# Optimization experiments

Measured on AMD Instinct MI355X. Metric: run time of the kernel, lower is better.

## Reference

```python
import jax, jax.numpy as jnp
import numpy as np

IN_DIM = 768
ATT_DIM = 512
N_HEADS = 8
HEAD_DIM = ATT_DIM // N_HEADS


def setup_inputs() -> dict:
    key = jax.random.key(0)
    k1, k2, k3 = jax.random.split(key, 3)
    X = jax.random.normal(k1, (4, 2048, IN_DIM), dtype=jnp.float32)
    # qkv linear (no bias): weight [3*att_dim, in_dim], torch convention y = x W^T
    W_qkv = jax.random.normal(k2, (3 * ATT_DIM, IN_DIM), dtype=jnp.float32) * (1.0 / np.sqrt(IN_DIM))
    W_out = jax.random.normal(k3, (IN_DIM, ATT_DIM), dtype=jnp.float32) * (1.0 / np.sqrt(ATT_DIM))
    b_out = jnp.zeros((IN_DIM,), dtype=jnp.float32)
    return {"X": X, "W_qkv": W_qkv, "W_out": W_out, "b_out": b_out}


def reference(X, W_qkv, W_out, b_out):
    b, n, _ = X.shape
    QKV = jnp.einsum('bnf,cf->bnc', X, W_qkv)  # [b, n, 3*att_dim]
    # rearrange 'b n (p h d) -> p b h n d'
    QKV = QKV.reshape(b, n, 3, N_HEADS, HEAD_DIM).transpose(2, 0, 3, 1, 4)
    Q, K, V = QKV[0], QKV[1], QKV[2]  # each [b, h, n, d]
    scores = jnp.einsum('bhid,bhjd->bhij', Q, K) / np.sqrt(HEAD_DIM)
    A = jax.nn.softmax(scores, axis=-1)  # dropout p=0 -> identity
    Y = jnp.einsum('bhij,bhjd->bhid', A, V)
    Y = Y.transpose(0, 2, 1, 3).reshape(b, n, ATT_DIM)  # 'b h n d -> b n (h d)'
    return jnp.einsum('bna,oa->bno', Y, W_out) + b_out
```

## Files before the change

### kernel.cpp

```cpp
#include <hip/hip_runtime.h>

typedef __bf16 bf16;
typedef unsigned int u32;
typedef __attribute__((ext_vector_type(8))) __bf16 bf16x8;
typedef __attribute__((ext_vector_type(4))) __bf16 bf16x4;
typedef __attribute__((ext_vector_type(4))) float floatx4;

#define IN_DIM  768
#define ATT_DIM 512
#define NH      8
#define HD      64
#define BATCH   4
#define SEQ     2048
#define M_TOT   (BATCH*SEQ)
#define QKV_N   (3*ATT_DIM)

#define QSCALE 0.18033688011112042f

__device__ __forceinline__ void cp16(void* lds, const void* g) {
    __builtin_amdgcn_global_load_lds((const __attribute__((address_space(1))) u32*)g,
                                     (__attribute__((address_space(3))) u32*)lds, 16, 0, 0);
}
__device__ __forceinline__ const bf16* swz(const bf16* b, int row, int chunk) {
    return b + row * 64 + (((chunk) ^ (row & 7)) << 3);
}

#define N8_X  (M_TOT * IN_DIM / 8)
#define N8_WQ (QKV_N * IN_DIM / 8)
#define N8_WO (IN_DIM * ATT_DIM / 8)
#define N8_ALL (N8_X + N8_WQ + N8_WO)

__global__ __launch_bounds__(256) void cvt_all(const float* __restrict__ X,
                                               const float* __restrict__ Wq,
                                               const float* __restrict__ Wo,
                                               bf16* __restrict__ Xb,
                                               bf16* __restrict__ Wqb,
                                               bf16* __restrict__ Wob) {
    int i = blockIdx.x * 256 + threadIdx.x;
    const float* s; bf16* d; int off;
    if (i < N8_X)            { s = X;  d = Xb;  off = i; }
    else if (i < N8_X+N8_WQ) { s = Wq; d = Wqb; off = i - N8_X; }
    else                     { s = Wo; d = Wob; off = i - N8_X - N8_WQ; }
    const float4 a = ((const float4*)s)[2*off];
    const float4 b = ((const float4*)s)[2*off+1];
    bf16x8 o = {(bf16)a.x,(bf16)a.y,(bf16)a.z,(bf16)a.w,
                (bf16)b.x,(bf16)b.y,(bf16)b.z,(bf16)b.w};
    ((bf16x8*)d)[off] = o;
}

__global__ __launch_bounds__(256) void qkv_gemm(const bf16* __restrict__ Xb,
                                                const bf16* __restrict__ Wb,
                                                bf16* __restrict__ Q,
                                                bf16* __restrict__ Kv,
                                                bf16* __restrict__ VT) {
    __shared__ __align__(16) char smraw[34816];
    bf16* As = (bf16*)smraw;
    bf16* Bs = (bf16*)(smraw + 16384);

    const int tid  = threadIdx.x;
    const int bm0  = blockIdx.y * 128;
    const int bn0  = blockIdx.x * 128;
    const int wave = tid >> 6, lane = tid & 63;
    const int quad = lane >> 4, l15 = lane & 15;
    const int wm = (wave >> 1) * 64, wn = (wave & 1) * 64;
    const int r8 = lane >> 3, cc = (lane & 7) ^ r8;

    const bf16* ag = Xb + (size_t)(bm0 + wave * 32 + r8) * IN_DIM + cc * 8;
    const bf16* bg = Wb + (size_t)(bn0 + wave * 32 + r8) * IN_DIM + cc * 8;

    floatx4 acc[4][4];
#pragma unroll
    for (int i = 0; i < 4; ++i)
#pragma unroll
        for (int j = 0; j < 4; ++j) acc[i][j] = (floatx4){0.f, 0.f, 0.f, 0.f};

    for (int kt = 0; kt < IN_DIM / 64; ++kt) {
        __syncthreads();
#pragma unroll
        for (int it = 0; it < 4; ++it) {
            cp16(&As[(wave * 32 + it * 8) * 64], ag + it * (8 * IN_DIM) + kt * 64);
            cp16(&Bs[(wave * 32 + it * 8) * 64], bg + it * (8 * IN_DIM) + kt * 64);
        }
        __syncthreads();

        bf16x8 af[2][4], bfr[2][4];
#pragma unroll
        for (int kh = 0; kh < 2; ++kh)
#pragma unroll
            for (int i = 0; i < 4; ++i) {
                af[kh][i]  = *(const bf16x8*)swz(As, wm + i * 16 + l15, kh * 4 + quad);
                bfr[kh][i] = *(const bf16x8*)swz(Bs, wn + i * 16 + l15, kh * 4 + quad);
            }
#pragma unroll
        for (int kh = 0; kh < 2; ++kh)
#pragma unroll
            for (int i = 0; i < 4; ++i)
#pragma unroll
                for (int j = 0; j < 4; ++j)
                    acc[i][j] = __builtin_amdgcn_mfma_f32_16x16x32_bf16(af[kh][i], bfr[kh][j], acc[i][j], 0, 0, 0);
    }

    const int b = bm0 >> 11, nbase = bm0 & 2047;

    if (bn0 < 1024) {
#pragma unroll
        for (int i = 0; i < 4; ++i)
#pragma unroll
            for (int j = 0; j < 4; ++j)
#pragma unroll
                for (int r = 0; r < 4; ++r) {
                    const int row = bm0 + wm + i * 16 + quad * 4 + r;
                    const int col = bn0 + wn + j * 16 + l15;
                    const float v = acc[i][j][r];
                    const int rem = col & 511;
                    const int h = rem >> 6, d = rem & 63;
                    const int n = row & 2047;
                    const size_t idx = (((size_t)((row >> 11) * NH + h)) * SEQ + n) * HD + d;
                    if (col < 512) Q[idx]  = (bf16)(v * QSCALE);
                    else           Kv[idx] = (bf16)v;
                }
    } else {
        __syncthreads();
        bf16 (*Ts)[136] = (bf16(*)[136])smraw;
#pragma unroll
        for (int i = 0; i < 4; ++i)
#pragma unroll
            for (int j = 0; j < 4; ++j) {
                bf16x4 pk = {(bf16)acc[i][j][0], (bf16)acc[i][j][1],
                             (bf16)acc[i][j][2], (bf16)acc[i][j][3]};
                *(bf16x4*)&Ts[wn + j * 16 + l15][wm + i * 16 + quad * 4] = pk;
            }
        __syncthreads();
        const int cb = bn0 - 1024;
#pragma unroll
        for (int t2 = 0; t2 < 8; ++t2) {
            const int id = tid + t2 * 256;
            const int c = id >> 4, nc = (id & 15) * 8;
            const int col = cb + c;
            const int h = col >> 6, d = col & 63;
            *(bf16x8*)&VT[(((size_t)(b * NH + h)) * HD + d) * SEQ + nbase + nc] =
                *(const bf16x8*)&Ts[c][nc];
        }
    }
}

__global__ __launch_bounds__(256, 4) void attn(const bf16* __restrict__ Q,
                                               const bf16* __restrict__ K,
                                               const bf16* __restrict__ VT,
                                               bf16* __restrict__ Y) {
    __shared__ bf16 Ks[2][64 * 64];
    __shared__ bf16 VTs[2][64 * 64];
    __shared__ bf16 Ps[4][16 * 64];

    const int tid  = threadIdx.x;
    const int wave = tid >> 6, lane = tid & 63;
    const int quad = lane >> 4, l15 = lane & 15;
    const int bh = blockIdx.x;
    const int q0 = blockIdx.y * 64;
    const bf16* Qg = Q  + (size_t)bh * SEQ * HD;
    const bf16* Kg = K  + (size_t)bh * SEQ * HD;
    const bf16* Vg = VT + (size_t)bh * HD * SEQ;

    const int r8 = lane >> 3, cc = (lane & 7) ^ r8;

    bf16x8 aq[2];
    aq[0] = *(const bf16x8*)&Qg[(size_t)(q0 + wave * 16 + l15) * 64 + quad * 8];
    aq[1] = *(const bf16x8*)&Qg[(size_t)(q0 + wave * 16 + l15) * 64 + 32 + quad * 8];

    const bf16* kg0 = Kg + (size_t)(wave * 16 + r8) * 64 + cc * 8;
    const bf16* kg1 = Kg + (size_t)(wave * 16 + 8 + r8) * 64 + cc * 8;
    const bf16* vg0 = Vg + (size_t)(wave * 16 + r8) * 2048 + cc * 8;
    const bf16* vg1 = Vg + (size_t)(wave * 16 + 8 + r8) * 2048 + cc * 8;

    cp16(&Ks[0][(wave * 16) * 64], kg0);
    cp16(&Ks[0][(wave * 16 + 8) * 64], kg1);
    cp16(&VTs[0][(wave * 16) * 64], vg0);
    cp16(&VTs[0][(wave * 16 + 8) * 64], vg1);

    float l = 0.f;
    floatx4 o[4];
#pragma unroll
    for (int db = 0; db < 4; ++db) o[db] = (floatx4){0.f, 0.f, 0.f, 0.f};

    bf16* psw = &Ps[wave][0];

    for (int kt = 0; kt < SEQ / 64; ++kt) {
        const int cur = kt & 1, nb = cur ^ 1;
        __syncthreads();
        if (kt < SEQ / 64 - 1) {
            cp16(&Ks[nb][(wave * 16) * 64], kg0 + (size_t)(kt + 1) * 4096);
            cp16(&Ks[nb][(wave * 16 + 8) * 64], kg1 + (size_t)(kt + 1) * 4096);
            cp16(&VTs[nb][(wave * 16) * 64], vg0 + (kt + 1) * 64);
            cp16(&VTs[nb][(wave * 16 + 8) * 64], vg1 + (kt + 1) * 64);
        }

#pragma unroll
        for (int t = 0; t < 4; ++t) {
            const int kr = t * 16 + l15;
            const bf16x8 k0 = *(const bf16x8*)swz(Ks[cur], kr, quad);
            const bf16x8 k1 = *(const bf16x8*)swz(Ks[cur], kr, 4 + quad);
            floatx4 z = (floatx4){0.f, 0.f, 0.f, 0.f};
            z = __builtin_amdgcn_mfma_f32_16x16x32_bf16(k0, aq[0], z, 0, 0, 0);
            z = __builtin_amdgcn_mfma_f32_16x16x32_bf16(k1, aq[1], z, 0, 0, 0);
            const float p0 = __builtin_amdgcn_exp2f(z[0]);
            const float p1 = __builtin_amdgcn_exp2f(z[1]);
            const float p2 = __builtin_amdgcn_exp2f(z[2]);
            const float p3 = __builtin_amdgcn_exp2f(z[3]);
            l += (p0 + p1) + (p2 + p3);
            bf16x4 pk = {(bf16)p0, (bf16)p1, (bf16)p2, (bf16)p3};
            const int c = t * 2 + (quad >> 1);
            *(bf16x4*)&psw[l15 * 64 + ((c ^ (l15 & 7)) << 3) + ((quad & 1) << 2)] = pk;
        }
        const bf16x8 pa0 = *(const bf16x8*)swz(psw, l15, quad);
        const bf16x8 pa1 = *(const bf16x8*)swz(psw, l15, 4 + quad);

#pragma unroll
        for (int db = 0; db < 4; ++db) {
            const int vr = db * 16 + l15;
            const bf16x8 v0 = *(const bf16x8*)swz(VTs[cur], vr, quad);
            const bf16x8 v1 = *(const bf16x8*)swz(VTs[cur], vr, 4 + quad);
            o[db] = __builtin_amdgcn_mfma_f32_16x16x32_bf16(pa0, v0, o[db], 0, 0, 0);
            o[db] = __builtin_amdgcn_mfma_f32_16x16x32_bf16(pa1, v1, o[db], 0, 0, 0);
        }
    }

    l += __shfl_xor(l, 16, 64);
    l += __shfl_xor(l, 32, 64);
    const float inv = 1.0f / l;
    float linv[4];
#pragma unroll
    for (int r = 0; r < 4; ++r)
        linv[r] = __int_as_float(__builtin_amdgcn_ds_bpermute((quad * 4 + r) * 4,
                                                              __float_as_int(inv)));
    const int b = bh >> 3, h = bh & 7;
#pragma unroll
    for (int db = 0; db < 4; ++db)
#pragma unroll
        for (int r = 0; r < 4; ++r) {
            const int n = q0 + wave * 16 + quad * 4 + r;
            Y[((size_t)(b * SEQ + n)) * ATT_DIM + h * HD + db * 16 + l15] =
                (bf16)(o[db][r] * linv[r]);
        }
}

__global__ __launch_bounds__(256) void out_gemm(const bf16* __restrict__ Yb,
                                                const bf16* __restrict__ Wb,
                                                const float* __restrict__ bias,
                                                float* __restrict__ out) {
    __shared__ __align__(16) bf16 As[128 * 64];
    __shared__ __align__(16) bf16 Bs[128 * 64];

    const int tid  = threadIdx.x;
    const int bm0  = blockIdx.y * 128;
    const int bn0  = blockIdx.x * 128;
    const int wave = tid >> 6, lane = tid & 63;
    const int quad = lane >> 4, l15 = lane & 15;
    const int wm = (wave >> 1) * 64, wn = (wave & 1) * 64;
    const int r8 = lane >> 3, cc = (lane & 7) ^ r8;

    const bf16* ag = Yb + (size_t)(bm0 + wave * 32 + r8) * ATT_DIM + cc * 8;
    const bf16* bg = Wb + (size_t)(bn0 + wave * 32 + r8) * ATT_DIM + cc * 8;

    floatx4 acc[4][4];
#pragma unroll
    for (int i = 0; i < 4; ++i)
#pragma unroll
        for (int j = 0; j < 4; ++j) acc[i][j] = (floatx4){0.f, 0.f, 0.f, 0.f};

    for (int kt = 0; kt < ATT_DIM / 64; ++kt) {
        __syncthreads();
#pragma unroll
        for (int it = 0; it < 4; ++it) {
            cp16(&As[(wave * 32 + it * 8) * 64], ag + it * (8 * ATT_DIM) + kt * 64);
            cp16(&Bs[(wave * 32 + it * 8) * 64], bg + it * (8 * ATT_DIM) + kt * 64);
        }
        __syncthreads();

        bf16x8 af[2][4], bfr[2][4];
#pragma unroll
        for (int kh = 0; kh < 2; ++kh)
#pragma unroll
            for (int i = 0; i < 4; ++i) {
                af[kh][i]  = *(const bf16x8*)swz(As, wm + i * 16 + l15, kh * 4 + quad);
                bfr[kh][i] = *(const bf16x8*)swz(Bs, wn + i * 16 + l15, kh * 4 + quad);
            }
#pragma unroll
        for (int kh = 0; kh < 2; ++kh)
#pragma unroll
            for (int i = 0; i < 4; ++i)
#pragma unroll
                for (int j = 0; j < 4; ++j)
                    acc[i][j] = __builtin_amdgcn_mfma_f32_16x16x32_bf16(af[kh][i], bfr[kh][j], acc[i][j], 0, 0, 0);
    }

#pragma unroll
    for (int i = 0; i < 4; ++i)
#pragma unroll
        for (int j = 0; j < 4; ++j)
#pragma unroll
            for (int r = 0; r < 4; ++r) {
                const int row = bm0 + wm + i * 16 + quad * 4 + r;
                const int col = bn0 + wn + j * 16 + l15;
                out[(size_t)row * IN_DIM + col] = acc[i][j][r] + bias[col];
            }
}

extern "C" void kernel_launch(void* const* d_in, const int* in_sizes, int n_in,
                              void* d_out, int out_size, void* d_ws, size_t ws_size,
                              hipStream_t stream) {
    const float* X    = (const float*)d_in[0];
    const float* Wqkv = (const float*)d_in[1];
    const float* Wout = (const float*)d_in[2];
    const float* bout = (const float*)d_in[3];
    float* out = (float*)d_out;

    char* ws = (char*)d_ws;
    size_t off = 0;
    bf16* Xb  = (bf16*)(ws + off); off += (size_t)M_TOT * IN_DIM * 2;
    bf16* Wqb = (bf16*)(ws + off); off += (size_t)QKV_N * IN_DIM * 2;
    bf16* Wob = (bf16*)(ws + off); off += (size_t)IN_DIM * ATT_DIM * 2;
    const size_t T = (size_t)BATCH * NH * SEQ * HD * 2;
    bf16* Q  = (bf16*)(ws + off); off += T;
    bf16* K  = (bf16*)(ws + off); off += T;
    bf16* VT = (bf16*)(ws + off); off += T;
    bf16* Y  = (bf16*)(ws + off); off += T;

    cvt_all<<<N8_ALL / 256, 256, 0, stream>>>(X, Wqkv, Wout, Xb, Wqb, Wob);
    qkv_gemm<<<dim3(QKV_N / 128, M_TOT / 128), 256, 0, stream>>>(Xb, Wqb, Q, K, VT);
    attn<<<dim3(BATCH * NH, SEQ / 64), 256, 0, stream>>>(Q, K, VT, Y);
    out_gemm<<<dim3(IN_DIM / 128, M_TOT / 128), 256, 0, stream>>>(Y, Wob, bout, out);
}
```

Measured before the change: 176.9 us.

## Process two query tiles per wave in attention; shrink out_gemm M tile

The attention kernel now gives each wave 32 query rows as two 16-row groups instead of 16, so every K and V^T tile staged in shared memory serves twice as many queries. This halves the grid and the global-to-LDS traffic for K/V per query. The cost is higher register pressure, with the launch-bounds occupancy hint lowered from 4 to 2 blocks per SM. Separately, out_gemm uses a 64x128 tile instead of 128x128, doubling its block count to give more parallelism on a small GEMM.

```diff
diff --git a/kernel.cpp b/kernel.cpp
--- a/kernel.cpp
+++ b/kernel.cpp
@@ -144,28 +144,32 @@
     }
 }
 
-__global__ __launch_bounds__(256, 4) void attn(const bf16* __restrict__ Q,
+__global__ __launch_bounds__(256, 2) void attn(const bf16* __restrict__ Q,
                                                const bf16* __restrict__ K,
                                                const bf16* __restrict__ VT,
                                                bf16* __restrict__ Y) {
     __shared__ bf16 Ks[2][64 * 64];
     __shared__ bf16 VTs[2][64 * 64];
-    __shared__ bf16 Ps[4][16 * 64];
+    __shared__ bf16 Ps[4][2][16 * 64];
 
     const int tid  = threadIdx.x;
     const int wave = tid >> 6, lane = tid & 63;
     const int quad = lane >> 4, l15 = lane & 15;
     const int bh = blockIdx.x;
-    const int q0 = blockIdx.y * 64;
+    const int q0 = blockIdx.y * 128;
     const bf16* Qg = Q  + (size_t)bh * SEQ * HD;
     const bf16* Kg = K  + (size_t)bh * SEQ * HD;
     const bf16* Vg = VT + (size_t)bh * HD * SEQ;
 
     const int r8 = lane >> 3, cc = (lane & 7) ^ r8;
 
-    bf16x8 aq[2];
-    aq[0] = *(const bf16x8*)&Qg[(size_t)(q0 + wave * 16 + l15) * 64 + quad * 8];
-    aq[1] = *(const bf16x8*)&Qg[(size_t)(q0 + wave * 16 + l15) * 64 + 32 + quad * 8];
+    bf16x8 aq[2][2];
+#pragma unroll
+    for (int g = 0; g < 2; ++g) {
+        const size_t qrow = (size_t)(q0 + wave * 32 + g * 16 + l15) * 64;
+        aq[g][0] = *(const bf16x8*)&Qg[qrow + quad * 8];
+        aq[g][1] = *(const bf16x8*)&Qg[qrow + 32 + quad * 8];
+    }
 
     const bf16* kg0 = Kg + (size_t)(wave * 16 + r8) * 64 + cc * 8;
     const bf16* kg1 = Kg + (size_t)(wave * 16 + 8 + r8) * 64 + cc * 8;
@@ -177,12 +181,12 @@
     cp16(&VTs[0][(wave * 16) * 64], vg0);
     cp16(&VTs[0][(wave * 16 + 8) * 64], vg1);
 
-    float l = 0.f;
-    floatx4 o[4];
-#pragma unroll
-    for (int db = 0; db < 4; ++db) o[db] = (floatx4){0.f, 0.f, 0.f, 0.f};
-
-    bf16* psw = &Ps[wave][0];
+    float l[2] = {0.f, 0.f};
+    floatx4 o[2][4];
+#pragma unroll
+    for (int g = 0; g < 2; ++g)
+#pragma unroll
+        for (int db = 0; db < 4; ++db) o[g][db] = (floatx4){0.f, 0.f, 0.f, 0.f};
 
     for (int kt = 0; kt < SEQ / 64; ++kt) {
         const int cur = kt & 1, nb = cur ^ 1;
@@ -199,102 +203,118 @@
             const int kr = t * 16 + l15;
             const bf16x8 k0 = *(const bf16x8*)swz(Ks[cur], kr, quad);
             const bf16x8 k1 = *(const bf16x8*)swz(Ks[cur], kr, 4 + quad);
-            floatx4 z = (floatx4){0.f, 0.f, 0.f, 0.f};
-            z = __builtin_amdgcn_mfma_f32_16x16x32_bf16(k0, aq[0], z, 0, 0, 0);
-            z = __builtin_amdgcn_mfma_f32_16x16x32_bf16(k1, aq[1], z, 0, 0, 0);
-            const float p0 = __builtin_amdgcn_exp2f(z[0]);
-            const float p1 = __builtin_amdgcn_exp2f(z[1]);
-            const float p2 = __builtin_amdgcn_exp2f(z[2]);
-            const float p3 = __builtin_amdgcn_exp2f(z[3]);
-            l += (p0 + p1) + (p2 + p3);
-            bf16x4 pk = {(bf16)p0, (bf16)p1, (bf16)p2, (bf16)p3};
             const int c = t * 2 + (quad >> 1);
-            *(bf16x4*)&psw[l15 * 64 + ((c ^ (l15 & 7)) << 3) + ((quad & 1) << 2)] = pk;
-        }
-        const bf16x8 pa0 = *(const bf16x8*)swz(psw, l15, quad);
-        const bf16x8 pa1 = *(const bf16x8*)swz(psw, l15, 4 + quad);
+            const int poff = l15 * 64 + ((c ^ (l15 & 7)) << 3) + ((quad & 1) << 2);
+#pragma unroll
+            for (int g = 0; g < 2; ++g) {
+                floatx4 z = (floatx4){0.f, 0.f, 0.f, 0.f};
+                z = __builtin_amdgcn_mfma_f32_16x16x32_bf16(k0, aq[g][0], z, 0, 0, 0);
+                z = __builtin_amdgcn_mfma_f32_16x16x32_bf16(k1, aq[g][1], z, 0, 0, 0);
+                const float p0 = __builtin_amdgcn_exp2f(z[0]);
+                const float p1 = __builtin_amdgcn_exp2f(z[1]);
+                const float p2 = __builtin_amdgcn_exp2f(z[2]);
+                const float p3 = __builtin_amdgcn_exp2f(z[3]);
+                l[g] += (p0 + p1) + (p2 + p3);
+                bf16x4 pk = {(bf16)p0, (bf16)p1, (bf16)p2, (bf16)p3};
+                *(bf16x4*)&Ps[wave][g][poff] = pk;
+            }
+        }
+        bf16x8 pa[2][2];
+#pragma unroll
+        for (int g = 0; g < 2; ++g) {
+            pa[g][0] = *(const bf16x8*)swz(&Ps[wave][g][0], l15, quad);
+            pa[g][1] = *(const bf16x8*)swz(&Ps[wave][g][0], l15, 4 + quad);
+        }
 
 #pragma unroll
         for (int db = 0; db < 4; ++db) {
             const int vr = db * 16 + l15;
             const bf16x8 v0 = *(const bf16x8*)swz(VTs[cur], vr, quad);
             const bf16x8 v1 = *(const bf16x8*)swz(VTs[cur], vr, 4 + quad);
-            o[db] = __builtin_amdgcn_mfma_f32_16x16x32_bf16(pa0, v0, o[db], 0, 0, 0);
-            o[db] = __builtin_amdgcn_mfma_f32_16x16x32_bf16(pa1, v1, o[db], 0, 0, 0);
-        }
-    }
-
-    l += __shfl_xor(l, 16, 64);
-    l += __shfl_xor(l, 32, 64);
-    const float inv = 1.0f / l;
-    float linv[4];
-#pragma unroll
-    for (int r = 0; r < 4; ++r)
-        linv[r] = __int_as_float(__builtin_amdgcn_ds_bpermute((quad * 4 + r) * 4,
-                                                              __float_as_int(inv)));
+#pragma unroll
+            for (int g = 0; g < 2; ++g) {
+                o[g][db] = __builtin_amdgcn_mfma_f32_16x16x32_bf16(pa[g][0], v0, o[g][db], 0, 0, 0);
+                o[g][db] = __builtin_amdgcn_mfma_f32_16x16x32_bf16(pa[g][1], v1, o[g][db], 0, 0, 0);
+            }
+        }
+    }
+
     const int b = bh >> 3, h = bh & 7;
 #pragma unroll
-    for (int db = 0; db < 4; ++db)
-#pragma unroll
-        for (int r = 0; r < 4; ++r) {
-            const int n = q0 + wave * 16 + quad * 4 + r;
-            Y[((size_t)(b * SEQ + n)) * ATT_DIM + h * HD + db * 16 + l15] =
-                (bf16)(o[db][r] * linv[r]);
-        }
+    for (int g = 0; g < 2; ++g) {
+        float lg = l[g];
+        lg += __shfl_xor(lg, 16, 64);
+        lg += __shfl_xor(lg, 32, 64);
+        const float inv = 1.0f / lg;
+        float linv[4];
+#pragma unroll
+        for (int r = 0; r < 4; ++r)
+            linv[r] = __int_as_float(__builtin_amdgcn_ds_bpermute((quad * 4 + r) * 4,
+                                                                  __float_as_int(inv)));
+#pragma unroll
+        for (int db = 0; db < 4; ++db)
+#pragma unroll
+            for (int r = 0; r < 4; ++r) {
+                const int n = q0 + wave * 32 + g * 16 + quad * 4 + r;
+                Y[((size_t)(b * SEQ + n)) * ATT_DIM + h * HD + db * 16 + l15] =
+                    (bf16)(o[g][db][r] * linv[r]);
+            }
+    }
 }
 
 __global__ __launch_bounds__(256) void out_gemm(const bf16* __restrict__ Yb,
                                                 const bf16* __restrict__ Wb,
                                                 const float* __restrict__ bias,
                                                 float* __restrict__ out) {
-    __shared__ __align__(16) bf16 As[128 * 64];
+    __shared__ __align__(16) bf16 As[64 * 64];
     __shared__ __align__(16) bf16 Bs[128 * 64];
 
     const int tid  = threadIdx.x;
-    const int bm0  = blockIdx.y * 128;
+    const int bm0  = blockIdx.y * 64;
     const int bn0  = blockIdx.x * 128;
     const int wave = tid >> 6, lane = tid & 63;
     const int quad = lane >> 4, l15 = lane & 15;
-    const int wm = (wave >> 1) * 64, wn = (wave & 1) * 64;
+    const int wm = (wave >> 1) * 32, wn = (wave & 1) * 64;
     const int r8 = lane >> 3, cc = (lane & 7) ^ r8;
 
-    const bf16* ag = Yb + (size_t)(bm0 + wave * 32 + r8) * ATT_DIM + cc * 8;
+    const bf16* ag = Yb + (size_t)(bm0 + wave * 16 + r8) * ATT_DIM + cc * 8;
     const bf16* bg = Wb + (size_t)(bn0 + wave * 32 + r8) * ATT_DIM + cc * 8;
 
-    floatx4 acc[4][4];
-#pragma unroll
-    for (int i = 0; i < 4; ++i)
+    floatx4 acc[2][4];
+#pragma unroll
+    for (int i = 0; i < 2; ++i)
 #pragma unroll
         for (int j = 0; j < 4; ++j) acc[i][j] = (floatx4){0.f, 0.f, 0.f, 0.f};
 
     for (int kt = 0; kt < ATT_DIM / 64; ++kt) {
         __syncthreads();
 #pragma unroll
-        for (int it = 0; it < 4; ++it) {
-            cp16(&As[(wave * 32 + it * 8) * 64], ag + it * (8 * ATT_DIM) + kt * 64);
+        for (int it = 0; it < 2; ++it)
+            cp16(&As[(wave * 16 + it * 8) * 64], ag + it * (8 * ATT_DIM) + kt * 64);
+#pragma unroll
+        for (int it = 0; it < 4; ++it)
             cp16(&Bs[(wave * 32 + it * 8) * 64], bg + it * (8 * ATT_DIM) + kt * 64);
-        }
-        __syncthreads();
-
-        bf16x8 af[2][4], bfr[2][4];
-#pragma unroll
-        for (int kh = 0; kh < 2; ++kh)
-#pragma unroll
-            for (int i = 0; i < 4; ++i) {
-                af[kh][i]  = *(const bf16x8*)swz(As, wm + i * 16 + l15, kh * 4 + quad);
-                bfr[kh][i] = *(const bf16x8*)swz(Bs, wn + i * 16 + l15, kh * 4 + quad);
-            }
-#pragma unroll
-        for (int kh = 0; kh < 2; ++kh)
-#pragma unroll
-            for (int i = 0; i < 4; ++i)
+        __syncthreads();
+
+#pragma unroll
+        for (int kh = 0; kh < 2; ++kh) {
+            bf16x8 af[2], bfr[4];
+#pragma unroll
+            for (int i = 0; i < 2; ++i)
+                af[i]  = *(const bf16x8*)swz(As, wm + i * 16 + l15, kh * 4 + quad);
+#pragma unroll
+            for (int j = 0; j < 4; ++j)
+                bfr[j] = *(const bf16x8*)swz(Bs, wn + j * 16 + l15, kh * 4 + quad);
+#pragma unroll
+            for (int i = 0; i < 2; ++i)
 #pragma unroll
                 for (int j = 0; j < 4; ++j)
-                    acc[i][j] = __builtin_amdgcn_mfma_f32_16x16x32_bf16(af[kh][i], bfr[kh][j], acc[i][j], 0, 0, 0);
-    }
-
-#pragma unroll
-    for (int i = 0; i < 4; ++i)
+                    acc[i][j] = __builtin_amdgcn_mfma_f32_16x16x32_bf16(af[i], bfr[j], acc[i][j], 0, 0, 0);
+        }
+    }
+
+#pragma unroll
+    for (int i = 0; i < 2; ++i)
 #pragma unroll
         for (int j = 0; j < 4; ++j)
 #pragma unroll
@@ -327,6 +347,6 @@
 
     cvt_all<<<N8_ALL / 256, 256, 0, stream>>>(X, Wqkv, Wout, Xb, Wqb, Wob);
     qkv_gemm<<<dim3(QKV_N / 128, M_TOT / 128), 256, 0, stream>>>(Xb, Wqb, Q, K, VT);
-    attn<<<dim3(BATCH * NH, SEQ / 64), 256, 0, stream>>>(Q, K, VT, Y);
-    out_gemm<<<dim3(IN_DIM / 128, M_TOT / 128), 256, 0, stream>>>(Y, Wob, bout, out);
-}
+    attn<<<dim3(BATCH * NH, SEQ / 128), 256, 0, stream>>>(Q, K, VT, Y);
+    out_gemm<<<dim3(IN_DIM / 128, M_TOT / 64), 256, 0, stream>>>(Y, Wob, bout, out);
+}
```

Result: no change. 178.5 us (+0.9%).
